# Optimization experiments

Hardware: AMD Instinct MI355X
Metric: run time of the kernel (lower is better)

## Reference

```python
import jax, jax.numpy as jnp
import numpy as np

B, N, E, H = 4, 1024, 1024, 16
D = E // H  # head_dim = 64

def setup_inputs() -> dict:
    key = jax.random.key(0)
    ks = jax.random.split(key, 6)
    s = 1.0 / np.sqrt(E)
    return {
        "query": jax.random.normal(ks[0], (B, N, E), jnp.float32),
        "key":   jax.random.normal(ks[1], (B, N, E), jnp.float32),
        "value": jax.random.normal(ks[2], (B, N, E), jnp.float32),
        "Wq": jax.random.normal(ks[3], (E, E), jnp.float32) * s,
        "Wk": jax.random.normal(ks[4], (E, E), jnp.float32) * s,
        "Wv": jax.random.normal(ks[5], (E, E), jnp.float32) * s,
    }

def reference(query, key, value, Wq, Wk, Wv):
    n = query.shape[1]
    # nn.Linear(bias=False): y = x @ W^T
    q = jnp.einsum('bne,fe->bnf', query, Wq)
    k = jnp.einsum('bne,fe->bnf', key, Wk)
    v = jnp.einsum('bne,fe->bnf', value, Wv)
    # Faithful to original: plain row-major reshape [B,n,H*D] -> [B*H,n,D]
    # (NOT a transpose-based head split).
    q = q.reshape(-1, n, D)
    k = k.reshape(-1, n, D)
    v = v.reshape(-1, n, D)
    a = jnp.einsum('gnd,gmd->gnm', q, k) / np.sqrt(D).astype(q.dtype)  # [B*H,n,n]
    a = jax.nn.softmax(a, axis=-1)
    out = jnp.einsum('gnm,gmd->gnd', a, v)        # [B*H,n,D]
    out = out.reshape(-1, n, H * D)               # [B,n,E]
    return out
```

## Files before the change

### kernel.cpp

```cpp
#include <hip/hip_runtime.h>
#include <stdint.h>

typedef unsigned short ushort_t;
typedef __attribute__((ext_vector_type(8))) short short8;
typedef __attribute__((ext_vector_type(4))) float f32x4;

#define OFF_QIN  0u
#define OFF_KIN  4194304u
#define OFF_VIN  8388608u
#define OFF_WQ   12582912u
#define OFF_WK   13631488u
#define OFF_WV   14680064u
#define OFF_QP   15728640u
#define OFF_KP   19922944u
#define OFF_VT   24117248u

__device__ __forceinline__ ushort_t f2bf(float f) {
  union { float f; unsigned u; } x; x.f = f;
  unsigned r = (x.u + 0x7fffu + ((x.u >> 16) & 1u)) >> 16;
  return (ushort_t)r;
}

__device__ __forceinline__ void gl_lds16(const void* g, void* l) {
  __builtin_amdgcn_global_load_lds(
      (const __attribute__((address_space(1))) void*)g,
      (__attribute__((address_space(3))) void*)l, 16, 0, 0);
}

__global__ void cvt_kernel(const float* __restrict__ q, const float* __restrict__ k,
                           const float* __restrict__ v, const float* __restrict__ wq,
                           const float* __restrict__ wk, const float* __restrict__ wv,
                           ushort_t* __restrict__ ws) {
  int cid = blockIdx.x * 256 + threadIdx.x;
  const float* src; int loc;
  if (cid < 1572864) {
    int seg = cid >> 19; loc = cid & 524287;
    src = (seg == 0) ? q : (seg == 1) ? k : v;
  } else {
    int c2 = cid - 1572864; int seg = c2 >> 17; loc = c2 & 131071;
    src = (seg == 0) ? wq : (seg == 1) ? wk : wv;
  }
  const float4* s4 = (const float4*)(src + (size_t)loc * 8);
  float4 a = s4[0], b = s4[1];
  short8 r;
  r[0] = f2bf(a.x); r[1] = f2bf(a.y); r[2] = f2bf(a.z); r[3] = f2bf(a.w);
  r[4] = f2bf(b.x); r[5] = f2bf(b.y); r[6] = f2bf(b.z); r[7] = f2bf(b.w);
  *(short8*)(ws + (size_t)cid * 8) = r;
}

__global__ __launch_bounds__(256) void gemm_qkv(ushort_t* __restrict__ ws) {
  int z = blockIdx.z;
  const ushort_t* A = ws + (z == 0 ? OFF_QIN : z == 1 ? OFF_KIN : OFF_VIN);
  const ushort_t* W = ws + (z == 0 ? OFF_WQ  : z == 1 ? OFF_WK  : OFF_WV);
  ushort_t* C       = ws + (z == 0 ? OFF_QP  : z == 1 ? OFF_KP  : OFF_VT);
  float scale = (z == 0) ? 0.18033688011112042f : 1.0f;

  __shared__ ushort_t As[128 * 32];
  __shared__ ushort_t Bs[128 * 32];

  int tid = threadIdx.x, lane = tid & 63, wv = tid >> 6;
  int wr = wv >> 1, wc = wv & 1;
  int r16 = lane & 15, kg = lane >> 4;
  int srow = lane >> 2;
  int scol = (lane & 3) * 8;

  int rowA0 = blockIdx.x * 128;
  int colB0 = blockIdx.y * 128;

  f32x4 acc[4][4];
#pragma unroll
  for (int m = 0; m < 4; m++)
#pragma unroll
    for (int n = 0; n < 4; n++) acc[m][n] = (f32x4){0.f, 0.f, 0.f, 0.f};

  for (int k0 = 0; k0 < 1024; k0 += 32) {
    __syncthreads();
#pragma unroll
    for (int r = 0; r < 2; r++) {
      int ch = wv * 2 + r;
      int row = ch * 16 + srow;
      gl_lds16(A + (size_t)(rowA0 + row) * 1024 + k0 + scol, &As[ch * 512]);
      gl_lds16(W + (size_t)(colB0 + row) * 1024 + k0 + scol, &Bs[ch * 512]);
    }
    __syncthreads();
    short8 af[4], bfr[4];
#pragma unroll
    for (int m = 0; m < 4; m++)
      af[m] = *(const short8*)&As[(wr * 64 + m * 16 + r16) * 32 + kg * 8];
#pragma unroll
    for (int n = 0; n < 4; n++)
      bfr[n] = *(const short8*)&Bs[(wc * 64 + n * 16 + r16) * 32 + kg * 8];
#pragma unroll
    for (int m = 0; m < 4; m++)
#pragma unroll
      for (int n = 0; n < 4; n++)
        acc[m][n] = __builtin_amdgcn_mfma_f32_16x16x32_bf16(af[m], bfr[n], acc[m][n], 0, 0, 0);
  }

  if (z < 2) {
#pragma unroll
    for (int m = 0; m < 4; m++)
#pragma unroll
      for (int n = 0; n < 4; n++) {
        int col = colB0 + wc * 64 + n * 16 + r16;
#pragma unroll
        for (int r = 0; r < 4; r++) {
          int row = rowA0 + wr * 64 + m * 16 + kg * 4 + r;
          C[(size_t)row * 1024 + col] = f2bf(acc[m][n][r] * scale);
        }
      }
  } else {
#pragma unroll
    for (int m = 0; m < 4; m++)
#pragma unroll
      for (int n = 0; n < 4; n++) {
        int col = colB0 + wc * 64 + n * 16 + r16;
        int h = col >> 6, d = col & 63;
#pragma unroll
        for (int r = 0; r < 4; r++) {
          int row = rowA0 + wr * 64 + m * 16 + kg * 4 + r;
          int b = row >> 10, nin = row & 1023;
          int g = b * 16 + (nin >> 6);
          int mseq = (nin & 63) * 16 + h;
          C[((size_t)g * 64 + d) * 1024 + mseq] = f2bf(acc[m][n][r]);
        }
      }
  }
}

__global__ __launch_bounds__(256) void attn_kernel(const ushort_t* __restrict__ ws,
                                                   float* __restrict__ out) {
  const ushort_t* Qp = ws + OFF_QP;
  const ushort_t* Kp = ws + OFF_KP;
  const ushort_t* Vt = ws + OFF_VT;

  __shared__ ushort_t Ks[64 * 72];
  __shared__ ushort_t Vs[64 * 72];
  __shared__ ushort_t Ps[4][16 * 72];

  int g = blockIdx.x;
  int qt = blockIdx.y;
  int b = g >> 4, cc = g & 15;
  int tid = threadIdx.x, lane = tid & 63, wv = tid >> 6;
  int r16 = lane & 15, kg = lane >> 4;

  short8 aq[2];
  {
    size_t base = ((size_t)(b * 1024 + cc * 64 + qt * 4 + wv)) * 1024 + r16 * 64;
    aq[0] = *(const short8*)&Qp[base + kg * 8];
    aq[1] = *(const short8*)&Qp[base + 32 + kg * 8];
  }

  f32x4 O[4];
#pragma unroll
  for (int i = 0; i < 4; i++) O[i] = (f32x4){0.f, 0.f, 0.f, 0.f};
  float mo[4] = {-1e30f, -1e30f, -1e30f, -1e30f};
  float lo[4] = {0.f, 0.f, 0.f, 0.f};

  int srr = tid >> 2;
  int sc0 = (tid & 3) * 16;
  const int nbase = b * 1024 + cc * 64;

  for (int it = 0; it < 16; it++) {
    __syncthreads();
    {
      size_t src = ((size_t)(nbase + it * 4 + (srr >> 4))) * 1024 + (srr & 15) * 64 + sc0;
      short8 v0 = *(const short8*)&Kp[src];
      short8 v1 = *(const short8*)&Kp[src + 8];
      *(short8*)&Ks[srr * 72 + sc0] = v0;
      *(short8*)&Ks[srr * 72 + sc0 + 8] = v1;
      size_t sv = ((size_t)g * 64 + srr) * 1024 + it * 64 + sc0;
      short8 w0 = *(const short8*)&Vt[sv];
      short8 w1 = *(const short8*)&Vt[sv + 8];
      *(short8*)&Vs[srr * 72 + sc0] = w0;
      *(short8*)&Vs[srr * 72 + sc0 + 8] = w1;
    }
    __syncthreads();

    f32x4 s[4];
#pragma unroll
    for (int jc = 0; jc < 4; jc++) {
      s[jc] = (f32x4){0.f, 0.f, 0.f, 0.f};
#pragma unroll
      for (int c2 = 0; c2 < 2; c2++) {
        short8 bk = *(const short8*)&Ks[(jc * 16 + r16) * 72 + c2 * 32 + kg * 8];
        s[jc] = __builtin_amdgcn_mfma_f32_16x16x32_bf16(aq[c2], bk, s[jc], 0, 0, 0);
      }
    }
    float mn[4], al[4], ls[4];
#pragma unroll
    for (int r = 0; r < 4; r++) {
      float mx = fmaxf(fmaxf(s[0][r], s[1][r]), fmaxf(s[2][r], s[3][r]));
#pragma unroll
      for (int off = 1; off < 16; off <<= 1) mx = fmaxf(mx, __shfl_xor(mx, off, 64));
      mn[r] = fmaxf(mo[r], mx);
      al[r] = exp2f(mo[r] - mn[r]);
      ls[r] = 0.f;
    }
#pragma unroll
    for (int jc = 0; jc < 4; jc++)
#pragma unroll
      for (int r = 0; r < 4; r++) {
        float p = exp2f(s[jc][r] - mn[r]);
        s[jc][r] = p;
        ls[r] += p;
      }
#pragma unroll
    for (int r = 0; r < 4; r++) {
#pragma unroll
      for (int off = 1; off < 16; off <<= 1) ls[r] += __shfl_xor(ls[r], off, 64);
      lo[r] = lo[r] * al[r] + ls[r];
      mo[r] = mn[r];
    }
#pragma unroll
    for (int dc = 0; dc < 4; dc++) {
      O[dc][0] *= al[0]; O[dc][1] *= al[1]; O[dc][2] *= al[2]; O[dc][3] *= al[3];
    }
#pragma unroll
    for (int jc = 0; jc < 4; jc++)
#pragma unroll
      for (int r = 0; r < 4; r++)
        Ps[wv][(kg * 4 + r) * 72 + jc * 16 + r16] = f2bf(s[jc][r]);
    short8 pa0 = *(const short8*)&Ps[wv][r16 * 72 + kg * 8];
    short8 pa1 = *(const short8*)&Ps[wv][r16 * 72 + 32 + kg * 8];
#pragma unroll
    for (int dc = 0; dc < 4; dc++) {
      short8 bv0 = *(const short8*)&Vs[(dc * 16 + r16) * 72 + kg * 8];
      O[dc] = __builtin_amdgcn_mfma_f32_16x16x32_bf16(pa0, bv0, O[dc], 0, 0, 0);
      short8 bv1 = *(const short8*)&Vs[(dc * 16 + r16) * 72 + 32 + kg * 8];
      O[dc] = __builtin_amdgcn_mfma_f32_16x16x32_bf16(pa1, bv1, O[dc], 0, 0, 0);
    }
  }

  size_t obase = ((size_t)(b * 1024 + cc * 64 + qt * 4 + wv)) * 1024;
#pragma unroll
  for (int r = 0; r < 4; r++) {
    float inv = 1.0f / lo[r];
#pragma unroll
    for (int dc = 0; dc < 4; dc++)
      out[obase + (kg * 4 + r) * 64 + dc * 16 + r16] = O[dc][r] * inv;
  }
}

extern "C" void kernel_launch(void* const* d_in, const int* in_sizes, int n_in,
                              void* d_out, int out_size, void* d_ws, size_t ws_size,
                              hipStream_t stream) {
  const float* q  = (const float*)d_in[0];
  const float* k  = (const float*)d_in[1];
  const float* v  = (const float*)d_in[2];
  const float* wq = (const float*)d_in[3];
  const float* wk = (const float*)d_in[4];
  const float* wv = (const float*)d_in[5];
  ushort_t* ws = (ushort_t*)d_ws;
  float* out = (float*)d_out;

  cvt_kernel<<<7680, 256, 0, stream>>>(q, k, v, wq, wk, wv, ws);
  dim3 gg(32, 8, 3);
  gemm_qkv<<<gg, 256, 0, stream>>>(ws);
  dim3 ga(64, 16);
  attn_kernel<<<ga, 256, 0, stream>>>(ws, out);
}
```

Baseline: 233.8 us.

## Restructure attention with transposed-S MFMA, lazy rescale, register P shuffle and separate V transpose

Moves the scattered V-transpose write out of the QKV GEMM epilogue into a dedicated LDS-based transpose kernel that reuses the dead Q-input workspace region. The attention kernel now processes 128-key tiles loaded via direct global-to-LDS copies into XOR-swizzled LDS, and computes S^T so each lane owns one query row, which removes the 16-lane shuffle reductions. It rescales the running max only when the new max exceeds the old by more than 8, and builds the bf16 P operand through register shuffles instead of an LDS round trip. The costs are an extra kernel launch and a more intricate lane permutation that is harder to verify.

```diff
diff --git a/kernel.cpp b/kernel.cpp
--- a/kernel.cpp
+++ b/kernel.cpp
@@ -4,7 +4,9 @@
 typedef unsigned short ushort_t;
 typedef __attribute__((ext_vector_type(8))) short short8;
 typedef __attribute__((ext_vector_type(4))) float f32x4;
-
+typedef __attribute__((ext_vector_type(4))) int int4v;
+
+#define OFF_VT   0u
 #define OFF_QIN  0u
 #define OFF_KIN  4194304u
 #define OFF_VIN  8388608u
@@ -13,7 +15,7 @@
 #define OFF_WV   14680064u
 #define OFF_QP   15728640u
 #define OFF_KP   19922944u
-#define OFF_VT   24117248u
+#define OFF_VP   24117248u
 
 __device__ __forceinline__ ushort_t f2bf(float f) {
   union { float f; unsigned u; } x; x.f = f;
@@ -32,34 +34,36 @@
                            const float* __restrict__ wk, const float* __restrict__ wv,
                            ushort_t* __restrict__ ws) {
   int cid = blockIdx.x * 256 + threadIdx.x;
-  const float* src; int loc;
+  const float* src; int loc; unsigned dstoff;
   if (cid < 1572864) {
     int seg = cid >> 19; loc = cid & 524287;
     src = (seg == 0) ? q : (seg == 1) ? k : v;
+    dstoff = (seg == 0) ? OFF_QIN : (seg == 1) ? OFF_KIN : OFF_VIN;
   } else {
     int c2 = cid - 1572864; int seg = c2 >> 17; loc = c2 & 131071;
     src = (seg == 0) ? wq : (seg == 1) ? wk : wv;
+    dstoff = (seg == 0) ? OFF_WQ : (seg == 1) ? OFF_WK : OFF_WV;
   }
   const float4* s4 = (const float4*)(src + (size_t)loc * 8);
   float4 a = s4[0], b = s4[1];
   short8 r;
   r[0] = f2bf(a.x); r[1] = f2bf(a.y); r[2] = f2bf(a.z); r[3] = f2bf(a.w);
   r[4] = f2bf(b.x); r[5] = f2bf(b.y); r[6] = f2bf(b.z); r[7] = f2bf(b.w);
-  *(short8*)(ws + (size_t)cid * 8) = r;
+  *(short8*)(ws + dstoff + (size_t)loc * 8) = r;
 }
 
 __global__ __launch_bounds__(256) void gemm_qkv(ushort_t* __restrict__ ws) {
   int z = blockIdx.z;
   const ushort_t* A = ws + (z == 0 ? OFF_QIN : z == 1 ? OFF_KIN : OFF_VIN);
   const ushort_t* W = ws + (z == 0 ? OFF_WQ  : z == 1 ? OFF_WK  : OFF_WV);
-  ushort_t* C       = ws + (z == 0 ? OFF_QP  : z == 1 ? OFF_KP  : OFF_VT);
+  ushort_t* C       = ws + (z == 0 ? OFF_QP  : z == 1 ? OFF_KP  : OFF_VP);
   float scale = (z == 0) ? 0.18033688011112042f : 1.0f;
 
   __shared__ ushort_t As[128 * 32];
   __shared__ ushort_t Bs[128 * 32];
 
-  int tid = threadIdx.x, lane = tid & 63, wv = tid >> 6;
-  int wr = wv >> 1, wc = wv & 1;
+  int tid = threadIdx.x, lane = tid & 63, wvid = tid >> 6;
+  int wr = wvid >> 1, wc = wvid & 1;
   int r16 = lane & 15, kg = lane >> 4;
   int srow = lane >> 2;
   int scol = (lane & 3) * 8;
@@ -77,7 +81,7 @@
     __syncthreads();
 #pragma unroll
     for (int r = 0; r < 2; r++) {
-      int ch = wv * 2 + r;
+      int ch = wvid * 2 + r;
       int row = ch * 16 + srow;
       gl_lds16(A + (size_t)(rowA0 + row) * 1024 + k0 + scol, &As[ch * 512]);
       gl_lds16(W + (size_t)(colB0 + row) * 1024 + k0 + scol, &Bs[ch * 512]);
@@ -97,35 +101,44 @@
         acc[m][n] = __builtin_amdgcn_mfma_f32_16x16x32_bf16(af[m], bfr[n], acc[m][n], 0, 0, 0);
   }
 
-  if (z < 2) {
-#pragma unroll
-    for (int m = 0; m < 4; m++)
-#pragma unroll
-      for (int n = 0; n < 4; n++) {
-        int col = colB0 + wc * 64 + n * 16 + r16;
-#pragma unroll
-        for (int r = 0; r < 4; r++) {
-          int row = rowA0 + wr * 64 + m * 16 + kg * 4 + r;
-          C[(size_t)row * 1024 + col] = f2bf(acc[m][n][r] * scale);
-        }
-      }
-  } else {
-#pragma unroll
-    for (int m = 0; m < 4; m++)
-#pragma unroll
-      for (int n = 0; n < 4; n++) {
-        int col = colB0 + wc * 64 + n * 16 + r16;
-        int h = col >> 6, d = col & 63;
-#pragma unroll
-        for (int r = 0; r < 4; r++) {
-          int row = rowA0 + wr * 64 + m * 16 + kg * 4 + r;
-          int b = row >> 10, nin = row & 1023;
-          int g = b * 16 + (nin >> 6);
-          int mseq = (nin & 63) * 16 + h;
-          C[((size_t)g * 64 + d) * 1024 + mseq] = f2bf(acc[m][n][r]);
-        }
-      }
-  }
+#pragma unroll
+  for (int m = 0; m < 4; m++)
+#pragma unroll
+    for (int n = 0; n < 4; n++) {
+      int col = colB0 + wc * 64 + n * 16 + r16;
+#pragma unroll
+      for (int r = 0; r < 4; r++) {
+        int row = rowA0 + wr * 64 + m * 16 + kg * 4 + r;
+        C[(size_t)row * 1024 + col] = f2bf(acc[m][n][r] * scale);
+      }
+    }
+}
+
+__global__ __launch_bounds__(256) void vtrans_kernel(ushort_t* __restrict__ ws) {
+  int bid = blockIdx.x;
+  int tc = bid & 3, c = (bid >> 2) & 15, b = bid >> 6;
+  __shared__ ushort_t T[16 * 1024];
+  const ushort_t* VP = ws + OFF_VP;
+  ushort_t* VT = ws + OFF_VT;
+  int tid = threadIdx.x;
+  size_t gbase = ((size_t)(b * 1024 + c * 64 + tc * 16)) * 1024;
+#pragma unroll
+  for (int i = 0; i < 8; i++) {
+    int L = (i * 256 + tid) * 8;
+    *(short8*)&T[L] = *(const short8*)&VP[gbase + L];
+  }
+  __syncthreads();
+  int d = tid & 63, sub = tid >> 6;
+  ushort_t tmp[64];
+#pragma unroll
+  for (int j = 0; j < 64; j++) {
+    int t = sub * 4 + (j >> 4), h = j & 15;
+    tmp[j] = T[t * 1024 + h * 64 + d];
+  }
+  size_t obase = ((size_t)((b * 16 + c) * 64 + d)) * 1024 + tc * 256 + sub * 64;
+#pragma unroll
+  for (int j = 0; j < 8; j++)
+    *(short8*)&VT[obase + j * 8] = *(short8*)&tmp[j * 8];
 }
 
 __global__ __launch_bounds__(256) void attn_kernel(const ushort_t* __restrict__ ws,
@@ -134,111 +147,142 @@
   const ushort_t* Kp = ws + OFF_KP;
   const ushort_t* Vt = ws + OFF_VT;
 
-  __shared__ ushort_t Ks[64 * 72];
-  __shared__ ushort_t Vs[64 * 72];
-  __shared__ ushort_t Ps[4][16 * 72];
+  __shared__ ushort_t Ks[128 * 64];
+  __shared__ ushort_t Vs[64 * 128];
 
   int g = blockIdx.x;
   int qt = blockIdx.y;
   int b = g >> 4, cc = g & 15;
-  int tid = threadIdx.x, lane = tid & 63, wv = tid >> 6;
+  int tid = threadIdx.x, lane = tid & 63, wvid = tid >> 6;
   int r16 = lane & 15, kg = lane >> 4;
+  int xr = r16 & 7;
+  const int nbase = b * 1024 + cc * 64;
 
   short8 aq[2];
   {
-    size_t base = ((size_t)(b * 1024 + cc * 64 + qt * 4 + wv)) * 1024 + r16 * 64;
+    size_t base = ((size_t)(nbase + qt * 4 + wvid)) * 1024 + r16 * 64;
     aq[0] = *(const short8*)&Qp[base + kg * 8];
     aq[1] = *(const short8*)&Qp[base + 32 + kg * 8];
   }
 
+  int koff[4], voff[4];
+#pragma unroll
+  for (int R = 0; R < 4; R++) {
+    int L = (R * 256 + tid) * 8;
+    koff[R] = (L & ~63) + ((((L >> 3) & 7) ^ ((L >> 6) & 7)) << 3);
+    voff[R] = (L >> 7) * 1024 + ((((L >> 3) & 15) ^ ((L >> 7) & 7)) << 3);
+  }
+  size_t kbase = (size_t)(nbase)*1024;
+  size_t vbase = (size_t)g * 65536;
+
   f32x4 O[4];
 #pragma unroll
   for (int i = 0; i < 4; i++) O[i] = (f32x4){0.f, 0.f, 0.f, 0.f};
-  float mo[4] = {-1e30f, -1e30f, -1e30f, -1e30f};
-  float lo[4] = {0.f, 0.f, 0.f, 0.f};
-
-  int srr = tid >> 2;
-  int sc0 = (tid & 3) * 16;
-  const int nbase = b * 1024 + cc * 64;
-
-  for (int it = 0; it < 16; it++) {
+  float mo = -1e30f, lo = 0.f;
+
+  for (int it = 0; it < 8; it++) {
     __syncthreads();
     {
-      size_t src = ((size_t)(nbase + it * 4 + (srr >> 4))) * 1024 + (srr & 15) * 64 + sc0;
-      short8 v0 = *(const short8*)&Kp[src];
-      short8 v1 = *(const short8*)&Kp[src + 8];
-      *(short8*)&Ks[srr * 72 + sc0] = v0;
-      *(short8*)&Ks[srr * 72 + sc0 + 8] = v1;
-      size_t sv = ((size_t)g * 64 + srr) * 1024 + it * 64 + sc0;
-      short8 w0 = *(const short8*)&Vt[sv];
-      short8 w1 = *(const short8*)&Vt[sv + 8];
-      *(short8*)&Vs[srr * 72 + sc0] = w0;
-      *(short8*)&Vs[srr * 72 + sc0 + 8] = w1;
+      size_t ktb = kbase + (size_t)it * 8192;
+      size_t vtb = vbase + (size_t)it * 128;
+#pragma unroll
+      for (int R = 0; R < 4; R++) {
+        gl_lds16(Kp + ktb + koff[R], &Ks[R * 2048 + wvid * 512]);
+        gl_lds16(Vt + vtb + voff[R], &Vs[R * 2048 + wvid * 512]);
+      }
     }
     __syncthreads();
 
-    f32x4 s[4];
-#pragma unroll
-    for (int jc = 0; jc < 4; jc++) {
+    f32x4 s[8];
+#pragma unroll
+    for (int jc = 0; jc < 8; jc++) {
       s[jc] = (f32x4){0.f, 0.f, 0.f, 0.f};
 #pragma unroll
       for (int c2 = 0; c2 < 2; c2++) {
-        short8 bk = *(const short8*)&Ks[(jc * 16 + r16) * 72 + c2 * 32 + kg * 8];
-        s[jc] = __builtin_amdgcn_mfma_f32_16x16x32_bf16(aq[c2], bk, s[jc], 0, 0, 0);
-      }
-    }
-    float mn[4], al[4], ls[4];
-#pragma unroll
-    for (int r = 0; r < 4; r++) {
-      float mx = fmaxf(fmaxf(s[0][r], s[1][r]), fmaxf(s[2][r], s[3][r]));
-#pragma unroll
-      for (int off = 1; off < 16; off <<= 1) mx = fmaxf(mx, __shfl_xor(mx, off, 64));
-      mn[r] = fmaxf(mo[r], mx);
-      al[r] = exp2f(mo[r] - mn[r]);
-      ls[r] = 0.f;
-    }
-#pragma unroll
-    for (int jc = 0; jc < 4; jc++)
+        short8 kf = *(const short8*)&Ks[(jc * 16 + r16) * 64 + (((c2 * 4 + kg) ^ xr) << 3)];
+        s[jc] = __builtin_amdgcn_mfma_f32_16x16x32_bf16(kf, aq[c2], s[jc], 0, 0, 0);
+      }
+    }
+
+    float tm = s[0][0];
+#pragma unroll
+    for (int jc = 0; jc < 8; jc++)
+#pragma unroll
+      for (int r = 0; r < 4; r++) tm = fmaxf(tm, s[jc][r]);
+    tm = fmaxf(tm, __shfl_xor(tm, 16));
+    tm = fmaxf(tm, __shfl_xor(tm, 32));
+
+    if (!__all(tm <= mo + 8.0f)) {
+      float mn = fmaxf(mo, tm);
+      float al = exp2f(mo - mn);
+#pragma unroll
+      for (int dc = 0; dc < 4; dc++) O[dc] = O[dc] * al;
+      lo *= al;
+      mo = mn;
+    }
+
+    float ls = 0.f;
+#pragma unroll
+    for (int jc = 0; jc < 8; jc++)
 #pragma unroll
       for (int r = 0; r < 4; r++) {
-        float p = exp2f(s[jc][r] - mn[r]);
-        s[jc][r] = p;
-        ls[r] += p;
-      }
-#pragma unroll
-    for (int r = 0; r < 4; r++) {
-#pragma unroll
-      for (int off = 1; off < 16; off <<= 1) ls[r] += __shfl_xor(ls[r], off, 64);
-      lo[r] = lo[r] * al[r] + ls[r];
-      mo[r] = mn[r];
-    }
-#pragma unroll
-    for (int dc = 0; dc < 4; dc++) {
-      O[dc][0] *= al[0]; O[dc][1] *= al[1]; O[dc][2] *= al[2]; O[dc][3] *= al[3];
-    }
-#pragma unroll
-    for (int jc = 0; jc < 4; jc++)
-#pragma unroll
-      for (int r = 0; r < 4; r++)
-        Ps[wv][(kg * 4 + r) * 72 + jc * 16 + r16] = f2bf(s[jc][r]);
-    short8 pa0 = *(const short8*)&Ps[wv][r16 * 72 + kg * 8];
-    short8 pa1 = *(const short8*)&Ps[wv][r16 * 72 + 32 + kg * 8];
-#pragma unroll
-    for (int dc = 0; dc < 4; dc++) {
-      short8 bv0 = *(const short8*)&Vs[(dc * 16 + r16) * 72 + kg * 8];
-      O[dc] = __builtin_amdgcn_mfma_f32_16x16x32_bf16(pa0, bv0, O[dc], 0, 0, 0);
-      short8 bv1 = *(const short8*)&Vs[(dc * 16 + r16) * 72 + 32 + kg * 8];
-      O[dc] = __builtin_amdgcn_mfma_f32_16x16x32_bf16(pa1, bv1, O[dc], 0, 0, 0);
-    }
-  }
-
-  size_t obase = ((size_t)(b * 1024 + cc * 64 + qt * 4 + wv)) * 1024;
-#pragma unroll
-  for (int r = 0; r < 4; r++) {
-    float inv = 1.0f / lo[r];
-#pragma unroll
-    for (int dc = 0; dc < 4; dc++)
-      out[obase + (kg * 4 + r) * 64 + dc * 16 + r16] = O[dc][r] * inv;
+        float pv = exp2f(s[jc][r] - mo);
+        s[jc][r] = pv;
+        ls += pv;
+      }
+    ls += __shfl_xor(ls, 16);
+    ls += __shfl_xor(ls, 32);
+    lo += ls;
+
+    int cp[8][2];
+#pragma unroll
+    for (int jc = 0; jc < 8; jc++) {
+#pragma unroll
+      for (int u = 0; u < 2; u++) {
+        int pk;
+        asm("v_cvt_pk_bf16_f32 %0, %1, %2" : "=v"(pk) : "v"(s[jc][2 * u]), "v"(s[jc][2 * u + 1]));
+        cp[jc][u] = pk;
+      }
+    }
+
+#pragma unroll
+    for (int kc = 0; kc < 4; kc++) {
+      int a0 = cp[2 * kc][0], a1 = cp[2 * kc][1];
+      int b0 = cp[2 * kc + 1][0], b1 = cp[2 * kc + 1][1];
+      int a0x = __shfl_xor(a0, 16), a1x = __shfl_xor(a1, 16);
+      int b0x = __shfl_xor(b0, 16), b1x = __shfl_xor(b1, 16);
+      bool lodd = (kg & 1);
+      int Aq0 = lodd ? a0x : a0, Aq1 = lodd ? a1x : a1;
+      int Aq2 = lodd ? a0 : a0x, Aq3 = lodd ? a1 : a1x;
+      int Bq0 = lodd ? b0x : b0, Bq1 = lodd ? b1x : b1;
+      int Bq2 = lodd ? b0 : b0x, Bq3 = lodd ? b1 : b1x;
+      bool hi = (kg >> 1) & 1;
+      int x0 = hi ? Aq0 : Bq0, x1 = hi ? Aq1 : Bq1;
+      int x2 = hi ? Aq2 : Bq2, x3 = hi ? Aq3 : Bq3;
+      int y0 = __shfl_xor(x0, 32), y1 = __shfl_xor(x1, 32);
+      int y2 = __shfl_xor(x2, 32), y3 = __shfl_xor(x3, 32);
+      int w0 = (kg == 0) ? Aq0 : (kg == 3) ? Bq0 : y0;
+      int w1 = (kg == 0) ? Aq1 : (kg == 3) ? Bq1 : y1;
+      int w2 = (kg == 0) ? Aq2 : (kg == 3) ? Bq2 : y2;
+      int w3 = (kg == 0) ? Aq3 : (kg == 3) ? Bq3 : y3;
+      int4v w; w[0] = w0; w[1] = w1; w[2] = w2; w[3] = w3;
+      short8 pf = *(short8*)&w;
+#pragma unroll
+      for (int dc = 0; dc < 4; dc++) {
+        short8 vf = *(const short8*)&Vs[(dc * 16 + r16) * 128 + (((kc * 4 + kg) ^ xr) << 3)];
+        O[dc] = __builtin_amdgcn_mfma_f32_16x16x32_bf16(vf, pf, O[dc], 0, 0, 0);
+      }
+    }
+  }
+
+  float inv = 1.0f / lo;
+  size_t obase = ((size_t)(nbase + qt * 4 + wvid)) * 1024 + r16 * 64;
+#pragma unroll
+  for (int dc = 0; dc < 4; dc++) {
+    float4 o4;
+    o4.x = O[dc][0] * inv; o4.y = O[dc][1] * inv;
+    o4.z = O[dc][2] * inv; o4.w = O[dc][3] * inv;
+    *(float4*)&out[obase + dc * 16 + kg * 4] = o4;
   }
 }
 
@@ -257,6 +301,7 @@
   cvt_kernel<<<7680, 256, 0, stream>>>(q, k, v, wq, wk, wv, ws);
   dim3 gg(32, 8, 3);
   gemm_qkv<<<gg, 256, 0, stream>>>(ws);
+  vtrans_kernel<<<256, 256, 0, stream>>>(ws);
   dim3 ga(64, 16);
   attn_kernel<<<ga, 256, 0, stream>>>(ws, out);
 }
```

Result: faster. 192.3 us (-17.7%).
